# Performance work log

Measured on AMD Instinct MI355X. Metric: run time of the kernel, lower is better.

Reference implementation:

```python
import jax, jax.numpy as jnp
import numpy as np

B, C, H, W, K = 16, 64, 256, 256, 3

def setup_inputs() -> dict:
    key = jax.random.key(0)
    ks = jax.random.split(key, 3)
    x = jax.random.normal(ks[0], (B, C, H, W), dtype=jnp.float32)
    # ReDistribution params
    rd_k = jnp.ones((1, C, 1, 1), jnp.float32)
    rd_b = jnp.zeros((1, C, 1, 1), jnp.float32)
    # Spectral binary activation beta
    beta = jnp.ones((1,), jnp.float32)
    # HardBinaryConv real-valued latent weights (Conv2d default init scale)
    fan_in = C * K * K
    bound = 1.0 / np.sqrt(fan_in)
    conv_w = jax.random.uniform(ks[1], (C, C, K, K), jnp.float32, -bound, bound)
    # RPReLU params
    pr_bias0 = jnp.zeros((1, C, 1, 1), jnp.float32)
    prelu_w = jnp.full((C,), 0.25, jnp.float32)
    pr_bias1 = jnp.zeros((1, C, 1, 1), jnp.float32)
    return {"x": x, "rd_k": rd_k, "rd_b": rd_b, "beta": beta,
            "conv_w": conv_w, "pr_bias0": pr_bias0, "prelu_w": prelu_w,
            "pr_bias1": pr_bias1}

def _ste(hard, soft):
    # straight-through estimator: forward=hard, backward grads flow via soft
    return jax.lax.stop_gradient(hard - soft) + soft

def reference(x, rd_k, rd_b, beta, conv_w, pr_bias0, prelu_w, pr_bias1):
    sg = jax.lax.stop_gradient
    # ReDistribution
    out = x * rd_k + rd_b
    # Spectral binary activation with tanh STE
    out = _ste(jnp.sign(out), jnp.tanh(out * beta))
    # HardBinaryConv: per-output-channel mean |w| scaling, sign binarize, clip STE
    scaling = sg(jnp.mean(jnp.abs(conv_w), axis=(1, 2, 3), keepdims=True))  # [C,1,1,1]
    bw = _ste(scaling * jnp.sign(conv_w), jnp.clip(conv_w, -1.0, 1.0))
    y = jax.lax.conv_general_dilated(
        out, bw, window_strides=(1, 1), padding=((1, 1), (1, 1)),
        dimension_numbers=("NCHW", "OIHW", "NCHW"))
    # RPReLU: bias0 -> per-channel PReLU -> bias1
    y = y + pr_bias0
    y = jnp.where(y >= 0, y, prelu_w[None, :, None, None] * y)
    y = y + pr_bias1
    return y + x
```

## Files before the change

### kernel.cpp

```cpp
#include <hip/hip_runtime.h>
#include <cstdint>
#include <cstddef>

#define Bn 16
#define Cn 64
#define Hn 256
#define Wn 256
#define HWn (Hn * Wn)
#define TH 8
#define ROWS (TH + 2)
#define COLS (Wn + 2)
#define NBLK (Bn * (Hn / TH))
#define THREADS 512

typedef unsigned long long u64;
typedef u64   u64x2 __attribute__((ext_vector_type(2)));
typedef float f32x4 __attribute__((ext_vector_type(4)));

__global__ __launch_bounds__(64) void pack_weights(const float* __restrict__ w,
                                                   const float* __restrict__ b0g,
                                                   const float* __restrict__ pwg,
                                                   const float* __restrict__ b1g,
                                                   u64* __restrict__ wbits,
                                                   float4* __restrict__ par,
                                                   int* __restrict__ corrx) {
    const int co = blockIdx.x;
    const int ci = threadIdx.x;
    const float* wp = w + ((size_t)co * Cn + ci) * 9;
    float v[9];
    float asum = 0.f;
    #pragma unroll
    for (int t = 0; t < 9; ++t) { v[t] = wp[t]; asum += fabsf(v[t]); }
    u64 m[9];
    #pragma unroll
    for (int t = 0; t < 9; ++t) m[t] = __ballot(v[t] > 0.f);
    #pragma unroll
    for (int off = 32; off; off >>= 1) asum += __shfl_xor(asum, off);
    if (ci == 0) {
        int c[9];
        #pragma unroll
        for (int t = 0; t < 9; ++t) {
            wbits[co * 9 + t] = m[t];
            c[t] = 64 - 2 * (int)__popcll(m[t]);
        }
        int* cx = corrx + co * 8;
        cx[0] = c[0] + c[1] + c[2];
        cx[1] = c[6] + c[7] + c[8];
        cx[2] = c[0] + c[3] + c[6];
        cx[3] = c[2] + c[5] + c[8];
        cx[4] = c[0]; cx[5] = c[2];
        cx[6] = c[6]; cx[7] = c[8];
        par[co] = make_float4(asum * (1.f / (Cn * 9)), b0g[co], pwg[co], b1g[co]);
    }
}

__global__ __launch_bounds__(THREADS, 4) void fused(const float* __restrict__ x,
                                                    const float* __restrict__ rdk,
                                                    const float* __restrict__ rdb,
                                                    const u64* __restrict__ wbits,
                                                    const float4* __restrict__ par,
                                                    const int* __restrict__ corrx,
                                                    float* __restrict__ out) {
    __shared__ __align__(16) u64 s_a[ROWS][COLS];
    __shared__ float2 s_rd[Cn];

    const int tid = threadIdx.x;
    const int bid     = blockIdx.x;
    const int logical = (bid & 7) * (NBLK / 8) + (bid >> 3);
    const int n  = logical >> 5;
    const int h0 = (logical & 31) * TH;

    if (tid < Cn) s_rd[tid] = make_float2(rdk[tid], rdb[tid]);
    if (tid < 2 * ROWS) s_a[tid >> 1][(tid & 1) ? (COLS - 1) : 0] = 0;
    __syncthreads();

    const float* xn = x + (size_t)n * Cn * HWn;
    for (int task = tid; task < 640; task += THREADS) {
        const int r  = task >> 6;
        const int q  = task & 63;
        const int gh = h0 - 1 + r;
        const int gw = 4 * q;
        u64 b0 = 0, b1 = 0, b2 = 0, b3 = 0;
        if (gh >= 0 && gh < Hn) {
            const float* xp = xn + (size_t)gh * Wn + gw;
            #pragma unroll 8
            for (int ci = 0; ci < Cn; ++ci) {
                const float2 kb = s_rd[ci];
                const f32x4 v = *reinterpret_cast<const f32x4*>(xp + (size_t)ci * HWn);
                const u64 bit = 1ull << ci;
                if (fmaf(v.x, kb.x, kb.y) > 0.f) b0 |= bit;
                if (fmaf(v.y, kb.x, kb.y) > 0.f) b1 |= bit;
                if (fmaf(v.z, kb.x, kb.y) > 0.f) b2 |= bit;
                if (fmaf(v.w, kb.x, kb.y) > 0.f) b3 |= bit;
            }
        }
        s_a[r][1 + gw] = b0;
        s_a[r][2 + gw] = b1;
        s_a[r][3 + gw] = b2;
        s_a[r][4 + gw] = b3;
    }
    __syncthreads();

    const int r  = tid >> 6;
    const int c0 = (tid & 63) * 4;
    const int h  = h0 + r;
    const int htop = (h == 0), hbot = (h == Hn - 1);
    const int wl = (c0 == 0), wr = (c0 + 3 == Wn - 1);
    const int need = htop | hbot | wl | wr;

    const float* xp = x   + (size_t)n * Cn * HWn + (size_t)h * Wn + c0;
    float*       op = out + (size_t)n * Cn * HWn + (size_t)h * Wn + c0;

    const u64* ap = &s_a[r][c0];
    for (int co0 = 0; co0 < Cn; co0 += 4) {
        asm volatile("" : "+v"(ap));
        u64 A[3][6];
        #pragma unroll
        for (int dh = 0; dh < 3; ++dh) {
            const u64x2 t0 = *reinterpret_cast<const u64x2*>(ap + dh * COLS);
            const u64x2 t1 = *reinterpret_cast<const u64x2*>(ap + dh * COLS + 2);
            const u64x2 t2 = *reinterpret_cast<const u64x2*>(ap + dh * COLS + 4);
            A[dh][0] = t0.x; A[dh][1] = t0.y; A[dh][2] = t1.x;
            A[dh][3] = t1.y; A[dh][4] = t2.x; A[dh][5] = t2.y;
        }
        #pragma unroll
        for (int dh = 0; dh < 3; ++dh)
            #pragma unroll
            for (int j = 0; j < 6; ++j)
                asm volatile("" : "+v"(A[dh][j]));

        f32x4 xq[4];
        #pragma unroll
        for (int j = 0; j < 4; ++j)
            xq[j] = *reinterpret_cast<const f32x4*>(xp + (size_t)(co0 + j) * HWn);

        #pragma unroll
        for (int j = 0; j < 4; ++j) {
            const int co = co0 + j;
            const u64* wb = wbits + co * 9;
            int is[4];
            #pragma unroll
            for (int p = 0; p < 4; ++p) {
                int acc = 0;
                #pragma unroll
                for (int dh = 0; dh < 3; ++dh) {
                    acc += (int)__popcll(A[dh][p]     ^ wb[dh * 3]);
                    acc += (int)__popcll(A[dh][p + 1] ^ wb[dh * 3 + 1]);
                    acc += (int)__popcll(A[dh][p + 2] ^ wb[dh * 3 + 2]);
                }
                is[p] = 576 - 2 * acc;
            }

            if (need) {
                const int* cx = corrx + co * 8;
                const int sb = (htop ? cx[0] : 0) + (hbot ? cx[1] : 0);
                #pragma unroll
                for (int p = 0; p < 4; ++p) is[p] -= sb;
                if (wl) is[0] -= cx[2] - (htop ? cx[4] : 0) - (hbot ? cx[6] : 0);
                if (wr) is[3] -= cx[3] - (htop ? cx[5] : 0) - (hbot ? cx[7] : 0);
            }

            const float4 p4 = par[co];
            f32x4 o;
            #pragma unroll
            for (int p = 0; p < 4; ++p) {
                float y = fmaf(p4.x, (float)is[p], p4.y);
                y = (y >= 0.f) ? y : y * p4.z;
                o[p] = y + p4.w + xq[j][p];
            }
            __builtin_nontemporal_store(o, reinterpret_cast<f32x4*>(op + (size_t)co * HWn));
        }
    }
}

extern "C" void kernel_launch(void* const* d_in, const int* in_sizes, int n_in,
                              void* d_out, int out_size, void* d_ws, size_t ws_size,
                              hipStream_t stream) {
    const float* x      = (const float*)d_in[0];
    const float* rd_k   = (const float*)d_in[1];
    const float* rd_b   = (const float*)d_in[2];
    const float* conv_w = (const float*)d_in[4];
    const float* pb0    = (const float*)d_in[5];
    const float* pw     = (const float*)d_in[6];
    const float* pb1    = (const float*)d_in[7];
    float* out = (float*)d_out;

    uint8_t* ws = (uint8_t*)d_ws;
    u64*    wbits = (u64*)ws;
    float4* par   = (float4*)(ws + 4608);
    int*    corrx = (int*)(ws + 4608 + 1024);

    pack_weights<<<Cn, 64, 0, stream>>>(conv_w, pb0, pw, pb1, wbits, par, corrx);
    fused<<<NBLK, THREADS, 0, stream>>>(x, rd_k, rd_b, wbits, par, corrx, out);
}
```

Measured before the change: 160.2 us.

## Overlap bit-packing of lower halo rows with first conv pass, one pixel per thread

```diff
diff --git a/kernel.cpp b/kernel.cpp
--- a/kernel.cpp
+++ b/kernel.cpp
@@ -11,10 +11,9 @@
 #define ROWS (TH + 2)
 #define COLS (Wn + 2)
 #define NBLK (Bn * (Hn / TH))
-#define THREADS 512
+#define THREADS 1024
 
 typedef unsigned long long u64;
-typedef u64   u64x2 __attribute__((ext_vector_type(2)));
 typedef float f32x4 __attribute__((ext_vector_type(4)));
 
 __global__ __launch_bounds__(64) void pack_weights(const float* __restrict__ w,
@@ -54,7 +53,7 @@
     }
 }
 
-__global__ __launch_bounds__(THREADS, 4) void fused(const float* __restrict__ x,
+__global__ __launch_bounds__(THREADS, 8) void fused(const float* __restrict__ x,
                                                     const float* __restrict__ rdk,
                                                     const float* __restrict__ rdb,
                                                     const u64* __restrict__ wbits,
@@ -75,9 +74,10 @@
     __syncthreads();
 
     const float* xn = x + (size_t)n * Cn * HWn;
-    for (int task = tid; task < 640; task += THREADS) {
-        const int r  = task >> 6;
-        const int q  = task & 63;
+
+    if (tid < 384) {
+        const int r  = tid >> 6;
+        const int q  = tid & 63;
         const int gh = h0 - 1 + r;
         const int gw = 4 * q;
         u64 b0 = 0, b1 = 0, b2 = 0, b3 = 0;
@@ -101,76 +101,111 @@
     }
     __syncthreads();
 
-    const int r  = tid >> 6;
-    const int c0 = (tid & 63) * 4;
-    const int h  = h0 + r;
-    const int htop = (h == 0), hbot = (h == Hn - 1);
-    const int wl = (c0 == 0), wr = (c0 + 3 == Wn - 1);
-    const int need = htop | hbot | wl | wr;
-
-    const float* xp = x   + (size_t)n * Cn * HWn + (size_t)h * Wn + c0;
-    float*       op = out + (size_t)n * Cn * HWn + (size_t)h * Wn + c0;
-
-    const u64* ap = &s_a[r][c0];
-    for (int co0 = 0; co0 < Cn; co0 += 4) {
-        asm volatile("" : "+v"(ap));
-        u64 A[3][6];
-        #pragma unroll
-        for (int dh = 0; dh < 3; ++dh) {
-            const u64x2 t0 = *reinterpret_cast<const u64x2*>(ap + dh * COLS);
-            const u64x2 t1 = *reinterpret_cast<const u64x2*>(ap + dh * COLS + 2);
-            const u64x2 t2 = *reinterpret_cast<const u64x2*>(ap + dh * COLS + 4);
-            A[dh][0] = t0.x; A[dh][1] = t0.y; A[dh][2] = t1.x;
-            A[dh][3] = t1.y; A[dh][4] = t2.x; A[dh][5] = t2.y;
-        }
+    const int r4 = tid >> 8;
+    const int c  = tid & 255;
+    const int wl = (c == 0), wr = (c == Wn - 1);
+
+    const bool packer = (tid < 256);
+    const int  prow = 6 + (tid >> 6);
+    const int  pgh  = h0 + 5 + (tid >> 6);
+    const int  pgw  = 4 * (tid & 63);
+    const bool pval = packer && (pgh < Hn);
+    const float* pxp = xn + (size_t)pgh * Wn + pgw;
+    u64 pb0 = 0, pb1 = 0, pb2 = 0, pb3 = 0;
+    f32x4 pend[4];
+
+    auto conv_pass = [&](int sr, int h, bool do_pack) {
+        const int htop = (h == 0), hbot = (h == Hn - 1);
+        const int need = htop | hbot | wl | wr;
+
+        u64 A[3][3];
         #pragma unroll
         for (int dh = 0; dh < 3; ++dh)
             #pragma unroll
-            for (int j = 0; j < 6; ++j)
-                asm volatile("" : "+v"(A[dh][j]));
-
-        f32x4 xq[4];
-        #pragma unroll
-        for (int j = 0; j < 4; ++j)
-            xq[j] = *reinterpret_cast<const f32x4*>(xp + (size_t)(co0 + j) * HWn);
-
-        #pragma unroll
-        for (int j = 0; j < 4; ++j) {
-            const int co = co0 + j;
-            const u64* wb = wbits + co * 9;
-            int is[4];
-            #pragma unroll
-            for (int p = 0; p < 4; ++p) {
+            for (int dw = 0; dw < 3; ++dw)
+                A[dh][dw] = s_a[sr + dh][c + dw];
+
+        const float* xp = xn + (size_t)h * Wn + c;
+        float*       op = out + (size_t)n * Cn * HWn + (size_t)h * Wn + c;
+
+        for (int i = 0; i < 16; ++i) {
+            if (do_pack && pval) {
+                if (i > 0) {
+                    #pragma unroll
+                    for (int k = 0; k < 4; ++k) {
+                        const int ci = 4 * (i - 1) + k;
+                        const float2 kb = s_rd[ci];
+                        const u64 bit = 1ull << ci;
+                        if (fmaf(pend[k].x, kb.x, kb.y) > 0.f) pb0 |= bit;
+                        if (fmaf(pend[k].y, kb.x, kb.y) > 0.f) pb1 |= bit;
+                        if (fmaf(pend[k].z, kb.x, kb.y) > 0.f) pb2 |= bit;
+                        if (fmaf(pend[k].w, kb.x, kb.y) > 0.f) pb3 |= bit;
+                    }
+                }
+                #pragma unroll
+                for (int k = 0; k < 4; ++k)
+                    pend[k] = *reinterpret_cast<const f32x4*>(pxp + (size_t)(4 * i + k) * HWn);
+            }
+
+            const int co0 = 4 * i;
+            float xq[4];
+            #pragma unroll
+            for (int j = 0; j < 4; ++j)
+                xq[j] = xp[(size_t)(co0 + j) * HWn];
+
+            #pragma unroll
+            for (int j = 0; j < 4; ++j) {
+                const int co = co0 + j;
+                const u64* wb = wbits + co * 9;
                 int acc = 0;
                 #pragma unroll
                 for (int dh = 0; dh < 3; ++dh) {
-                    acc += (int)__popcll(A[dh][p]     ^ wb[dh * 3]);
-                    acc += (int)__popcll(A[dh][p + 1] ^ wb[dh * 3 + 1]);
-                    acc += (int)__popcll(A[dh][p + 2] ^ wb[dh * 3 + 2]);
+                    acc += (int)__popcll(A[dh][0] ^ wb[dh * 3]);
+                    acc += (int)__popcll(A[dh][1] ^ wb[dh * 3 + 1]);
+                    acc += (int)__popcll(A[dh][2] ^ wb[dh * 3 + 2]);
                 }
-                is[p] = 576 - 2 * acc;
-            }
-
-            if (need) {
-                const int* cx = corrx + co * 8;
-                const int sb = (htop ? cx[0] : 0) + (hbot ? cx[1] : 0);
-                #pragma unroll
-                for (int p = 0; p < 4; ++p) is[p] -= sb;
-                if (wl) is[0] -= cx[2] - (htop ? cx[4] : 0) - (hbot ? cx[6] : 0);
-                if (wr) is[3] -= cx[3] - (htop ? cx[5] : 0) - (hbot ? cx[7] : 0);
-            }
-
-            const float4 p4 = par[co];
-            f32x4 o;
-            #pragma unroll
-            for (int p = 0; p < 4; ++p) {
-                float y = fmaf(p4.x, (float)is[p], p4.y);
+                int is = 576 - 2 * acc;
+
+                if (need) {
+                    const int* cx = corrx + co * 8;
+                    is -= (htop ? cx[0] : 0) + (hbot ? cx[1] : 0);
+                    if (wl) is -= cx[2] - (htop ? cx[4] : 0) - (hbot ? cx[6] : 0);
+                    if (wr) is -= cx[3] - (htop ? cx[5] : 0) - (hbot ? cx[7] : 0);
+                }
+
+                const float4 p4 = par[co];
+                float y = fmaf(p4.x, (float)is, p4.y);
                 y = (y >= 0.f) ? y : y * p4.z;
-                o[p] = y + p4.w + xq[j][p];
-            }
-            __builtin_nontemporal_store(o, reinterpret_cast<f32x4*>(op + (size_t)co * HWn));
-        }
+                __builtin_nontemporal_store(y + p4.w + xq[j],
+                                            op + (size_t)co * HWn);
+            }
+        }
+
+        if (do_pack && pval) {
+            #pragma unroll
+            for (int k = 0; k < 4; ++k) {
+                const int ci = 60 + k;
+                const float2 kb = s_rd[ci];
+                const u64 bit = 1ull << ci;
+                if (fmaf(pend[k].x, kb.x, kb.y) > 0.f) pb0 |= bit;
+                if (fmaf(pend[k].y, kb.x, kb.y) > 0.f) pb1 |= bit;
+                if (fmaf(pend[k].z, kb.x, kb.y) > 0.f) pb2 |= bit;
+                if (fmaf(pend[k].w, kb.x, kb.y) > 0.f) pb3 |= bit;
+            }
+        }
+    };
+
+    conv_pass(r4, h0 + r4, true);
+
+    if (packer) {
+        s_a[prow][1 + pgw] = pb0;
+        s_a[prow][2 + pgw] = pb1;
+        s_a[prow][3 + pgw] = pb2;
+        s_a[prow][4 + pgw] = pb3;
     }
+    __syncthreads();
+
+    conv_pass(r4 + 4, h0 + 4 + r4, false);
 }
 
 extern "C" void kernel_launch(void* const* d_in, const int* in_sizes, int n_in,
```

Result: slower. 234.3 us (+46.3%).
